# Kernel tuning notes

Measured on AMD Instinct MI355X. Metric: run time of the kernel, lower is better.

Reference implementation:

```python
import jax, jax.numpy as jnp
import numpy as np

N_NODES = 100000
N_EDGES = 1600000
IN_FEATS = 128
HIDDEN = 128
N_CLASSES = 40
EPS = 1e-5  # BatchNorm1d default eps


def setup_inputs():
    key = jax.random.key(0)
    ks = jax.random.split(key, 12)
    s_in = 1.0 / np.sqrt(IN_FEATS)
    s_h = 1.0 / np.sqrt(HIDDEN)
    return {
        "feat": jax.random.normal(ks[0], (N_NODES, IN_FEATS), jnp.float32),
        "src": jax.random.randint(ks[1], (N_EDGES,), 0, N_NODES, jnp.int32),
        "dst": jax.random.randint(ks[2], (N_EDGES,), 0, N_NODES, jnp.int32),
        # GraphConv weights, stored (out, in) as in the torch module
        "w0": jax.random.normal(ks[3], (HIDDEN, IN_FEATS), jnp.float32) * s_in,
        "w1": jax.random.normal(ks[4], (HIDDEN, HIDDEN), jnp.float32) * s_h,
        "w2": jax.random.normal(ks[5], (N_CLASSES, HIDDEN), jnp.float32) * s_h,
        "b2": jnp.zeros((N_CLASSES,), jnp.float32),  # bias only on last layer
        # skip-connection linears (use_linear=True, bias=False)
        "l0": jax.random.normal(ks[6], (HIDDEN, IN_FEATS), jnp.float32) * s_in,
        "l1": jax.random.normal(ks[7], (HIDDEN, HIDDEN), jnp.float32) * s_h,
        "l2": jax.random.normal(ks[8], (N_CLASSES, HIDDEN), jnp.float32) * s_h,
        # BatchNorm affine params for the two hidden layers
        "g0": jnp.ones((HIDDEN,), jnp.float32),
        "beta0": jnp.zeros((HIDDEN,), jnp.float32),
        "g1": jnp.ones((HIDDEN,), jnp.float32),
        "beta1": jnp.zeros((HIDDEN,), jnp.float32),
    }


def _spmm(h, src, dst):
    # copy_u + sum aggregation: out[d] = sum_{e: dst[e]==d} h[src[e]]
    return jax.ops.segment_sum(h[src], dst, num_segments=N_NODES)


def gcn_forward(feat, src, dst, w0, w1, w2, b2, l0, l1, l2, g0, beta0, g1, beta1):
    ones = jnp.ones((src.shape[0],), jnp.float32)
    out_deg = jnp.clip(jax.ops.segment_sum(ones, src, num_segments=N_NODES), 1.0)
    in_deg = jnp.clip(jax.ops.segment_sum(ones, dst, num_segments=N_NODES), 1.0)
    out_norm = out_deg ** -0.5  # norm='both', applied to src features
    in_norm = in_deg ** -0.5    # norm='both', applied to aggregated result

    def conv(h, W, bias, in_gt_out):
        hs = h * out_norm[:, None]
        if in_gt_out:  # in_feats > out_feats: project first, then aggregate
            rst = _spmm(hs @ W.T, src, dst)
        else:          # aggregate first, then project
            rst = _spmm(hs, src, dst) @ W.T
        rst = rst * in_norm[:, None]
        if bias is not None:
            rst = rst + bias
        return rst

    def bn(x, g, b):
        mu = x.mean(0)
        var = x.var(0)  # biased variance, matches BN training-mode normalization
        return (x - mu) * jax.lax.rsqrt(var + EPS) * g + b

    h = feat  # dropout in eval mode = identity
    h = jax.nn.relu(bn(conv(h, w0, None, IN_FEATS > HIDDEN) + h @ l0.T, g0, beta0))
    h = jax.nn.relu(bn(conv(h, w1, None, False) + h @ l1.T, g1, beta1))
    h = conv(h, w2, b2, HIDDEN > N_CLASSES) + h @ l2.T
    return h


def reference(feat, src, dst, w0, w1, w2, b2, l0, l1, l2, g0, beta0, g1, beta1):
    return gcn_forward(feat, src, dst, w0, w1, w2, b2, l0, l1, l2, g0, beta0, g1, beta1)
```

## Files before the change

### kernel.cpp

```cpp
#include <hip/hip_runtime.h>
#include <hip/hip_fp16.h>
#include <cstdint>
#include <cstddef>

#define N_NODES 100000
#define N_EDGES 1600000
#define EPS 1e-5f

typedef _Float16 half8 __attribute__((ext_vector_type(8)));
typedef float floatx4 __attribute__((ext_vector_type(4)));

#define HCH 64
#define HRG 4
#define HBINS 32768
#define HWORDS (HBINS / 2)
#define HCHUNK (N_EDGES / HCH)
#define HCHUNK4 (HCHUNK / 4)

__global__ void k_hist_part(const int* __restrict__ keys, unsigned int* __restrict__ Hpart) {
  __shared__ unsigned int bins[HWORDS];
  int c = blockIdx.x % HCH, r = blockIdx.x / HCH;
  int base = r * HBINS;
  for (int i = threadIdx.x; i < HWORDS; i += 256) bins[i] = 0;
  __syncthreads();
  const int4* k4 = (const int4*)(keys + c * HCHUNK);
  for (int i = threadIdx.x; i < HCHUNK4; i += 256) {
    int4 k = k4[i];
    int a;
    a = k.x - base; if ((unsigned)a < (unsigned)HBINS) atomicAdd(&bins[a >> 1], 1u << ((a & 1) * 16));
    a = k.y - base; if ((unsigned)a < (unsigned)HBINS) atomicAdd(&bins[a >> 1], 1u << ((a & 1) * 16));
    a = k.z - base; if ((unsigned)a < (unsigned)HBINS) atomicAdd(&bins[a >> 1], 1u << ((a & 1) * 16));
    a = k.w - base; if ((unsigned)a < (unsigned)HBINS) atomicAdd(&bins[a >> 1], 1u << ((a & 1) * 16));
  }
  __syncthreads();
  unsigned int* outp = Hpart + ((size_t)blockIdx.x << 14);
  for (int i = threadIdx.x; i < HWORDS; i += 256) outp[i] = bins[i];
}

__global__ void k_hist_scan2(const unsigned short* __restrict__ Hs,
                             unsigned short* __restrict__ Hd,
                             int* __restrict__ degd, float* __restrict__ out_norm,
                             float* __restrict__ in_norm, int* __restrict__ bsum) {
  __shared__ int sred[256];
  int t = threadIdx.x;
  int b = blockIdx.x * 256 + t;
  int total = 0;
  if (b < N_NODES) {
    int r = b >> 15, lo = b & (HBINS - 1);
    const unsigned short* ps = Hs + ((size_t)(r * HCH) << 15) + lo;
    unsigned int ds = 0;
#pragma unroll 8
    for (int c = 0; c < HCH; ++c) ds += ps[(size_t)c << 15];
    unsigned short* pd = Hd + ((size_t)(r * HCH) << 15) + lo;
    unsigned int tt = 0;
#pragma unroll 8
    for (int c = 0; c < HCH; ++c) {
      unsigned int v = pd[(size_t)c << 15];
      pd[(size_t)c << 15] = (unsigned short)tt;
      tt += v;
    }
    total = (int)tt;
    degd[b] = total;
    out_norm[b] = rsqrtf((float)max((int)ds, 1));
    in_norm[b] = rsqrtf((float)max(total, 1));
  }
  sred[t] = total;
  __syncthreads();
  for (int off = 128; off > 0; off >>= 1) {
    if (t < off) sred[t] += sred[t + off];
    __syncthreads();
  }
  if (t == 0) bsum[blockIdx.x] = sred[0];
}

__global__ void k_build(const int* __restrict__ src, const int* __restrict__ dst,
                        const unsigned short* __restrict__ Hbase,
                        const int* __restrict__ row_start, int* __restrict__ col) {
  __shared__ unsigned int cur[HWORDS];
  int c = blockIdx.x % HCH, r = blockIdx.x / HCH;
  int base = r * HBINS;
  for (int i = threadIdx.x; i < HWORDS; i += 256) cur[i] = 0;
  __syncthreads();
  const unsigned short* hb = Hbase + ((size_t)blockIdx.x << 15);
  const int4* d4 = (const int4*)(dst + c * HCHUNK);
  const int4* s4 = (const int4*)(src + c * HCHUNK);
  for (int i = threadIdx.x; i < HCHUNK4; i += 256) {
    int4 d = d4[i];
    int4 s = s4[i];
    int a;
    a = d.x - base;
    if ((unsigned)a < (unsigned)HBINS) {
      unsigned old = atomicAdd(&cur[a >> 1], 1u << ((a & 1) * 16));
      unsigned lr = (old >> ((a & 1) * 16)) & 0xffffu;
      col[row_start[d.x] + hb[a] + lr] = s.x;
    }
    a = d.y - base;
    if ((unsigned)a < (unsigned)HBINS) {
      unsigned old = atomicAdd(&cur[a >> 1], 1u << ((a & 1) * 16));
      unsigned lr = (old >> ((a & 1) * 16)) & 0xffffu;
      col[row_start[d.y] + hb[a] + lr] = s.y;
    }
    a = d.z - base;
    if ((unsigned)a < (unsigned)HBINS) {
      unsigned old = atomicAdd(&cur[a >> 1], 1u << ((a & 1) * 16));
      unsigned lr = (old >> ((a & 1) * 16)) & 0xffffu;
      col[row_start[d.z] + hb[a] + lr] = s.z;
    }
    a = d.w - base;
    if ((unsigned)a < (unsigned)HBINS) {
      unsigned old = atomicAdd(&cur[a >> 1], 1u << ((a & 1) * 16));
      unsigned lr = (old >> ((a & 1) * 16)) & 0xffffu;
      col[row_start[d.w] + hb[a] + lr] = s.w;
    }
  }
}

__global__ void k_scan2(int* bsum, int nb) {
  __shared__ int s[512];
  int t = threadIdx.x;
  int v = (t < nb) ? bsum[t] : 0;
  s[t] = v;
  __syncthreads();
  for (int off = 1; off < 512; off <<= 1) {
    int x = (t >= off) ? s[t - off] : 0;
    __syncthreads();
    s[t] += x;
    __syncthreads();
  }
  if (t < nb) bsum[t] = s[t] - v;
}

__global__ void k_scan3(const int* __restrict__ degd, const int* __restrict__ bsum,
                        int* row_start) {
  __shared__ int s[256];
  int t = threadIdx.x;
  int i = blockIdx.x * 256 + t;
  int v = (i < N_NODES) ? degd[i] : 0;
  s[t] = v;
  __syncthreads();
  for (int off = 1; off < 256; off <<= 1) {
    int x = (t >= off) ? s[t - off] : 0;
    __syncthreads();
    s[t] += x;
    __syncthreads();
  }
  if (i < N_NODES) row_start[i] = bsum[blockIdx.x] + s[t] - v;
  if (i == 0) row_start[N_NODES] = N_EDGES;
}

__global__ void k_w2h(const float* __restrict__ w0, const float* __restrict__ l0,
                      const float* __restrict__ w1, const float* __restrict__ l1,
                      const float* __restrict__ w2, const float* __restrict__ l2,
                      unsigned short* __restrict__ W) {
  int i = blockIdx.x * 256 + threadIdx.x;
  if (i >= 18944) return;
  int h = i * 4;
  const float* src; int off;
  if (h < 16384)      { src = w0; off = h; }
  else if (h < 32768) { src = l0; off = h - 16384; }
  else if (h < 49152) { src = w1; off = h - 32768; }
  else if (h < 65536) { src = l1; off = h - 49152; }
  else if (h < 70656) { src = w2; off = h - 65536; }
  else                { src = l2; off = h - 70656; }
  float4 v = *(const float4*)(src + off);
  ushort4 o;
  o.x = __half_as_ushort(__float2half_rn(v.x));
  o.y = __half_as_ushort(__float2half_rn(v.y));
  o.z = __half_as_ushort(__float2half_rn(v.z));
  o.w = __half_as_ushort(__float2half_rn(v.w));
  ((ushort4*)W)[i] = o;
}

__global__ void k_feat2h(const float* __restrict__ feat, unsigned short* __restrict__ F) {
  int i = blockIdx.x * 256 + threadIdx.x;
  if (i >= N_NODES * 32) return;
  float4 v = ((const float4*)feat)[i];
  ushort4 u;
  u.x = __half_as_ushort(__float2half_rn(v.x));
  u.y = __half_as_ushort(__float2half_rn(v.y));
  u.z = __half_as_ushort(__float2half_rn(v.z));
  u.w = __half_as_ushort(__float2half_rn(v.w));
  ((ushort4*)F)[i] = u;
}

template<int BN>
__global__ void k_agg128h(const unsigned short* __restrict__ X, const int* __restrict__ col,
                          const int* __restrict__ row_start,
                          const float* __restrict__ out_norm,
                          const float* __restrict__ in_norm,
                          const float* __restrict__ stats,
                          const float* __restrict__ g, const float* __restrict__ bb,
                          unsigned short* __restrict__ out16) {
  __shared__ float scA[128], shA[128];
  int t = threadIdx.x;
  if (BN) {
    if (t < 128) {
      const float inv = 1.f / (float)N_NODES;
      float mu = stats[t] * inv;
      float var = stats[128 + t] * inv - mu * mu;
      float s = rsqrtf(var + EPS) * g[t];
      scA[t] = s;
      shA[t] = bb[t] - mu * s;
    }
    __syncthreads();
  }
  int wave = t >> 6;
  int lane = t & 63;
  int node = blockIdx.x * 4 + wave;
  if (node >= N_NODES) return;
  int q = lane >> 4;
  int sub = lane & 15;
  float scR[8], shR[8];
  if (BN) {
#pragma unroll
    for (int j = 0; j < 8; ++j) { scR[j] = scA[sub * 8 + j]; shR[j] = shA[sub * 8 + j]; }
  }
  int s0 = row_start[node], s1 = row_start[node + 1];
  const uint4* hp = (const uint4*)X;
  float a[8];
#pragma unroll
  for (int j = 0; j < 8; ++j) a[j] = 0.f;
  int e = s0 + q;
  for (; e + 4 < s1; e += 8) {
    int c0 = col[e];
    int c1 = col[e + 4];
    float on0 = out_norm[c0];
    float on1 = out_norm[c1];
    uint4 u0 = hp[(size_t)c0 * 16 + sub];
    uint4 u1 = hp[(size_t)c1 * 16 + sub];
    const __half2* h0 = (const __half2*)&u0;
    const __half2* h1 = (const __half2*)&u1;
#pragma unroll
    for (int j = 0; j < 4; ++j) {
      float2 f0 = __half22float2(h0[j]);
      float2 f1 = __half22float2(h1[j]);
      if (BN) {
        f0.x = fmaxf(f0.x * scR[2 * j] + shR[2 * j], 0.f);
        f0.y = fmaxf(f0.y * scR[2 * j + 1] + shR[2 * j + 1], 0.f);
        f1.x = fmaxf(f1.x * scR[2 * j] + shR[2 * j], 0.f);
        f1.y = fmaxf(f1.y * scR[2 * j + 1] + shR[2 * j + 1], 0.f);
      }
      a[2 * j] += on0 * f0.x + on1 * f1.x;
      a[2 * j + 1] += on0 * f0.y + on1 * f1.y;
    }
  }
  if (e < s1) {
    int c = col[e];
    float on = out_norm[c];
    uint4 u = hp[(size_t)c * 16 + sub];
    const __half2* h0 = (const __half2*)&u;
#pragma unroll
    for (int j = 0; j < 4; ++j) {
      float2 f = __half22float2(h0[j]);
      if (BN) {
        f.x = fmaxf(f.x * scR[2 * j] + shR[2 * j], 0.f);
        f.y = fmaxf(f.y * scR[2 * j + 1] + shR[2 * j + 1], 0.f);
      }
      a[2 * j] += on * f.x;
      a[2 * j + 1] += on * f.y;
    }
  }
#pragma unroll
  for (int j = 0; j < 8; ++j) {
    a[j] += __shfl_xor(a[j], 16);
    a[j] += __shfl_xor(a[j], 32);
  }
  if (q == 0) {
    float sc = in_norm[node];
    __half2 o[4];
#pragma unroll
    for (int j = 0; j < 4; ++j)
      o[j] = __float22half2_rn(make_float2(a[2 * j] * sc, a[2 * j + 1] * sc));
    ((uint4*)out16)[(size_t)node * 16 + sub] = *(const uint4*)o;
  }
}

template<int BN>
__launch_bounds__(256)
__global__ void k_gemm_dual16(const unsigned short* __restrict__ Xa,
                              const unsigned short* __restrict__ Xh,
                              const float* __restrict__ stats,
                              const float* __restrict__ g, const float* __restrict__ bb,
                              const unsigned short* __restrict__ W16,
                              unsigned short* __restrict__ Out16, float* __restrict__ pstats) {
  __shared__ __align__(16) unsigned short smem[128 * 136];
  __shared__ float scA[128], shA[128];
  int t = threadIdx.x;
  int row0 = blockIdx.x * 64;
  int w = t >> 6, lane = t & 63;
  int q = lane >> 4, m = lane & 15;
  if (BN && t < 128) {
    const float inv = 1.f / (float)N_NODES;
    float mu = stats[t] * inv;
    float var = stats[128 + t] * inv - mu * mu;
    float s = rsqrtf(var + EPS) * g[t];
    scA[t] = s;
    shA[t] = bb[t] - mu * s;
  }
  size_t arow = (size_t)min(row0 + w * 16 + m, N_NODES - 1);
  floatx4 acc[8];
#pragma unroll
  for (int i = 0; i < 8; ++i) acc[i] = (floatx4){0.f, 0.f, 0.f, 0.f};

  for (int phase = 0; phase < 2; ++phase) {
    const unsigned short* Xg = phase ? Xh : Xa;
    const uint4* xr = (const uint4*)Xg + arow * 16 + q;
    uint4 av[4];
    av[0] = xr[0]; av[1] = xr[4]; av[2] = xr[8]; av[3] = xr[12];
    __syncthreads();
    {
      const uint4* wsrc = (const uint4*)(W16 + ((size_t)phase << 14));
#pragma unroll
      for (int it = 0; it < 8; ++it) {
        int idx = it * 256 + t;
        *(uint4*)&smem[(idx >> 4) * 136 + (idx & 15) * 8] = wsrc[idx];
      }
    }
    if (BN && phase == 1) {
#pragma unroll
      for (int ks = 0; ks < 4; ++ks) {
        int kk = ks * 32 + q * 8;
        __half2* hh = (__half2*)&av[ks];
#pragma unroll
        for (int j = 0; j < 4; ++j) {
          float2 f = __half22float2(hh[j]);
          f.x = fmaxf(f.x * scA[kk + 2 * j] + shA[kk + 2 * j], 0.f);
          f.y = fmaxf(f.y * scA[kk + 2 * j + 1] + shA[kk + 2 * j + 1], 0.f);
          hh[j] = __float22half2_rn(f);
        }
      }
    }
    __syncthreads();
#pragma unroll
    for (int ks = 0; ks < 4; ++ks) {
      half8 a = *(half8*)&av[ks];
      int kk = ks * 32 + q * 8;
#pragma unroll
      for (int t8 = 0; t8 < 8; ++t8) {
        half8 b = *(const half8*)&smem[(t8 * 16 + m) * 136 + kk];
        acc[t8] = __builtin_amdgcn_mfma_f32_16x16x32_f16(a, b, acc[t8], 0, 0, 0);
      }
    }
  }
  float ps[8], pq[8];
#pragma unroll
  for (int t8 = 0; t8 < 8; ++t8) {
    float s = 0.f, sq = 0.f;
#pragma unroll
    for (int i = 0; i < 4; ++i) {
      int row = row0 + w * 16 + q * 4 + i;
      if (row < N_NODES) {
        float v = acc[t8][i];
        s += v; sq += v * v;
      }
    }
    s += __shfl_xor(s, 16);
    s += __shfl_xor(s, 32);
    sq += __shfl_xor(sq, 16);
    sq += __shfl_xor(sq, 32);
    ps[t8] = s; pq[t8] = sq;
  }
  __syncthreads();
  unsigned short* sT = smem;
  float* pSum = (float*)(smem + 8704);
  float* pSq = pSum + 512;
#pragma unroll
  for (int t8 = 0; t8 < 8; ++t8) {
    int c = t8 * 16 + m;
#pragma unroll
    for (int i = 0; i < 4; ++i) {
      int r = w * 16 + q * 4 + i;
      sT[r * 136 + c] = __half_as_ushort(__float2half_rn(acc[t8][i]));
    }
    if (q == 0) {
      pSum[w * 128 + c] = ps[t8];
      pSq[w * 128 + c] = pq[t8];
    }
  }
  __syncthreads();
#pragma unroll
  for (int it = 0; it < 4; ++it) {
    int idx = it * 256 + t;
    int r = idx >> 4, gg = idx & 15;
    int row = row0 + r;
    if (row < N_NODES)
      *(uint4*)&Out16[(size_t)row * 128 + gg * 8] = *(const uint4*)&sT[r * 136 + gg * 8];
  }
  if (t < 128) {
    float s = (pSum[t] + pSum[128 + t]) + (pSum[256 + t] + pSum[384 + t]);
    float sq = (pSq[t] + pSq[128 + t]) + (pSq[256 + t] + pSq[384 + t]);
    pstats[(size_t)blockIdx.x * 256 + t] = s;
    pstats[(size_t)blockIdx.x * 256 + 128 + t] = sq;
  }
}

__global__ void k_stats_red(const float* __restrict__ pstats, float* __restrict__ stats,
                            int nblk) {
  int t = threadIdx.x;
  float s = 0.f;
  for (int b = blockIdx.x; b < nblk; b += gridDim.x)
    s += pstats[(size_t)b * 256 + t];
  atomicAdd(&stats[t], s);
}

__launch_bounds__(256)
__global__ void k_gemm2_16(const unsigned short* __restrict__ X,
                           const float* __restrict__ stats,
                           const float* __restrict__ g, const float* __restrict__ bb,
                           const unsigned short* __restrict__ W80,
                           const float* __restrict__ b2,
                           const float* __restrict__ out_norm,
                           __half* __restrict__ p, float* __restrict__ out) {
  __shared__ __align__(16) unsigned short smem[80 * 136];
  __shared__ float scA[128], shA[128];
  int t = threadIdx.x;
  int row0 = blockIdx.x * 64;
  int w = t >> 6, lane = t & 63;
  int q = lane >> 4, m = lane & 15;
  if (t < 128) {
    const float inv = 1.f / (float)N_NODES;
    float mu = stats[t] * inv;
    float var = stats[128 + t] * inv - mu * mu;
    float s = rsqrtf(var + EPS) * g[t];
    scA[t] = s;
    shA[t] = bb[t] - mu * s;
  }
  size_t arow = (size_t)min(row0 + w * 16 + m, N_NODES - 1);
  const uint4* xr = (const uint4*)X + arow * 16 + q;
  uint4 av[4];
  av[0] = xr[0]; av[1] = xr[4]; av[2] = xr[8]; av[3] = xr[12];
  {
    const uint4* wsrc = (const uint4*)W80;
#pragma unroll
    for (int it = 0; it < 5; ++it) {
      int idx = it * 256 + t;
      *(uint4*)&smem[(idx >> 4) * 136 + (idx & 15) * 8] = wsrc[idx];
    }
  }
  __syncthreads();
#pragma unroll
  for (int ks = 0; ks < 4; ++ks) {
    int kk = ks * 32 + q * 8;
    __half2* hh = (__half2*)&av[ks];
#pragma unroll
    for (int j = 0; j < 4; ++j) {
      float2 f = __half22float2(hh[j]);
      f.x = fmaxf(f.x * scA[kk + 2 * j] + shA[kk + 2 * j], 0.f);
      f.y = fmaxf(f.y * scA[kk + 2 * j + 1] + shA[kk + 2 * j + 1], 0.f);
      hh[j] = __float22half2_rn(f);
    }
  }
  floatx4 acc[5];
#pragma unroll
  for (int i = 0; i < 5; ++i) acc[i] = (floatx4){0.f, 0.f, 0.f, 0.f};
#pragma unroll
  for (int ks = 0; ks < 4; ++ks) {
    half8 a = *(half8*)&av[ks];
    int kk = ks * 32 + q * 8;
#pragma unroll
    for (int t5 = 0; t5 < 5; ++t5) {
      half8 b = *(const half8*)&smem[(t5 * 16 + m) * 136 + kk];
      acc[t5] = __builtin_amdgcn_mfma_f32_16x16x32_f16(a, b, acc[t5], 0, 0, 0);
    }
  }
  __syncthreads();
  unsigned short* sTp = smem;
  float* sTo = (float*)(smem + 4608);
  {
    unsigned int* zp = (unsigned int*)sTp;
    for (int idx = t; idx < 768; idx += 256) {
      int r = idx / 12, wc = 20 + idx % 12;
      zp[r * 36 + wc] = 0u;
    }
  }
  float on4[4];
#pragma unroll
  for (int i = 0; i < 4; ++i) {
    int row = row0 + w * 16 + q * 4 + i;
    on4[i] = out_norm[min(row, N_NODES - 1)];
  }
#pragma unroll
  for (int t5 = 0; t5 < 5; ++t5) {
    int c = t5 * 16 + m;
#pragma unroll
    for (int i = 0; i < 4; ++i) {
      int r = w * 16 + q * 4 + i;
      if (c < 40) {
        sTp[r * 72 + c] = __half_as_ushort(__float2half_rn(on4[i] * acc[t5][i]));
      } else {
        sTo[r * 44 + (c - 40)] = acc[t5][i] + b2[c - 40];
      }
    }
  }
  __syncthreads();
#pragma unroll
  for (int it = 0; it < 2; ++it) {
    int idx = it * 256 + t;
    int r = idx >> 3, gg = idx & 7;
    int row = row0 + r;
    if (row < N_NODES)
      *(uint4*)((unsigned short*)p + (size_t)row * 64 + gg * 8) = *(const uint4*)&sTp[r * 72 + gg * 8];
  }
  for (int it = 0; it < 3; ++it) {
    int idx = it * 256 + t;
    if (idx < 640) {
      int r = idx / 10, gg = idx % 10;
      int row = row0 + r;
      if (row < N_NODES)
        *(float4*)(out + (size_t)row * 40 + gg * 4) = *(const float4*)&sTo[r * 44 + gg * 4];
    }
  }
}

__global__ void k_agg64h(const __half* __restrict__ p, const int* __restrict__ col,
                         const int* __restrict__ row_start,
                         const float* __restrict__ in_norm,
                         float* __restrict__ out) {
  int wave = threadIdx.x >> 6, lane = threadIdx.x & 63;
  int node = blockIdx.x * 4 + wave;
  if (node >= N_NODES) return;
  int oct = lane >> 3;
  int sub = lane & 7;
  int s0 = row_start[node], s1 = row_start[node + 1];
  const uint4* pp = (const uint4*)p;
  float a[8];
#pragma unroll
  for (int j = 0; j < 8; ++j) a[j] = 0.f;
  int e = s0 + oct;
  for (; e + 8 < s1; e += 16) {
    int c0 = col[e];
    int c1 = col[e + 8];
    uint4 u0 = pp[(size_t)c0 * 8 + sub];
    uint4 u1 = pp[(size_t)c1 * 8 + sub];
    const __half2* h0 = (const __half2*)&u0;
    const __half2* h1 = (const __half2*)&u1;
#pragma unroll
    for (int j = 0; j < 4; ++j) {
      float2 f0 = __half22float2(h0[j]);
      float2 f1 = __half22float2(h1[j]);
      a[2 * j] += f0.x + f1.x;
      a[2 * j + 1] += f0.y + f1.y;
    }
  }
  if (e < s1) {
    uint4 u = pp[(size_t)col[e] * 8 + sub];
    const __half2* h0 = (const __half2*)&u;
#pragma unroll
    for (int j = 0; j < 4; ++j) {
      float2 f = __half22float2(h0[j]);
      a[2 * j] += f.x;
      a[2 * j + 1] += f.y;
    }
  }
#pragma unroll
  for (int j = 0; j < 8; ++j) {
    a[j] += __shfl_xor(a[j], 8);
    a[j] += __shfl_xor(a[j], 16);
    a[j] += __shfl_xor(a[j], 32);
  }
  if (oct == 0 && sub < 5) {
    float sc = in_norm[node];
    float4* op = (float4*)(out + (size_t)node * 40 + (size_t)sub * 8);
    float4 v0 = op[0], v1 = op[1];
    v0.x += sc * a[0]; v0.y += sc * a[1]; v0.z += sc * a[2]; v0.w += sc * a[3];
    v1.x += sc * a[4]; v1.y += sc * a[5]; v1.z += sc * a[6]; v1.w += sc * a[7];
    op[0] = v0; op[1] = v1;
  }
}

extern "C" void kernel_launch(void* const* d_in, const int* in_sizes, int n_in,
                              void* d_out, int out_size, void* d_ws, size_t ws_size,
                              hipStream_t stream) {
  const float* feat = (const float*)d_in[0];
  const int* src = (const int*)d_in[1];
  const int* dst = (const int*)d_in[2];
  const float* w0 = (const float*)d_in[3];
  const float* w1 = (const float*)d_in[4];
  const float* w2 = (const float*)d_in[5];
  const float* b2 = (const float*)d_in[6];
  const float* l0 = (const float*)d_in[7];
  const float* l1 = (const float*)d_in[8];
  const float* l2 = (const float*)d_in[9];
  const float* g0 = (const float*)d_in[10];
  const float* beta0 = (const float*)d_in[11];
  const float* g1 = (const float*)d_in[12];
  const float* beta1 = (const float*)d_in[13];
  float* out = (float*)d_out;

  char* ws = (char*)d_ws;
  size_t off = 0;
  auto alloc = [&](size_t bytes) {
    void* ptr = ws + off;
    off = (off + bytes + 255) & ~(size_t)255;
    return ptr;
  };
  unsigned short* A16 = (unsigned short*)alloc(2 * (size_t)N_NODES * 128);
  float* B = (float*)alloc(sizeof(float) * (size_t)N_NODES * 128);
  unsigned short* F = (unsigned short*)alloc(2 * (size_t)N_NODES * 128);
  int* degd = (int*)alloc(sizeof(int) * N_NODES);
  int* row_start = (int*)alloc(sizeof(int) * (N_NODES + 1));
  int* colb = (int*)alloc(sizeof(int) * N_EDGES);
  float* out_norm = (float*)alloc(sizeof(float) * N_NODES);
  float* in_norm = (float*)alloc(sizeof(float) * N_NODES);
  int* bsum = (int*)alloc(sizeof(int) * 512);
  float* stats0 = (float*)alloc(sizeof(float) * 256);
  float* stats1 = (float*)alloc(sizeof(float) * 256);
  unsigned short* W16 = (unsigned short*)alloc(2 * (size_t)75776);
  int gb = (N_NODES + 63) / 64;
  float* pstats = (float*)alloc(sizeof(float) * (size_t)gb * 256);

  unsigned int* Hs = (unsigned int*)B;
  unsigned int* Hd = Hs + (size_t)HCH * HRG * HWORDS;
  unsigned short* P0 = (unsigned short*)B;
  unsigned short* P1 = F;

  int nb = (N_NODES + 255) / 256;
  int hb = HCH * HRG;

  k_w2h<<<74, 256, 0, stream>>>(w0, l0, w1, l1, w2, l2, W16);

  k_hist_part<<<hb, 256, 0, stream>>>(src, Hs);
  k_hist_part<<<hb, 256, 0, stream>>>(dst, Hd);
  k_hist_scan2<<<nb, 256, 0, stream>>>((const unsigned short*)Hs, (unsigned short*)Hd,
                                       degd, out_norm, in_norm, bsum);
  k_scan2<<<1, 512, 0, stream>>>(bsum, nb);
  k_scan3<<<nb, 256, 0, stream>>>(degd, bsum, row_start);
  k_build<<<hb, 256, 0, stream>>>(src, dst, (const unsigned short*)Hd, row_start, colb);

  int ab = (N_NODES + 3) / 4;
  int fb = (N_NODES * 32 + 255) / 256;

  k_feat2h<<<fb, 256, 0, stream>>>(feat, F);
  k_agg128h<0><<<ab, 256, 0, stream>>>(F, colb, row_start, out_norm, in_norm,
                                       nullptr, nullptr, nullptr, A16);
  k_gemm_dual16<0><<<gb, 256, 0, stream>>>(A16, F, nullptr, nullptr, nullptr,
                                           W16, P0, pstats);
  hipMemsetAsync(stats0, 0, sizeof(float) * 256, stream);
  k_stats_red<<<32, 256, 0, stream>>>(pstats, stats0, gb);

  k_agg128h<1><<<ab, 256, 0, stream>>>(P0, colb, row_start, out_norm, in_norm,
                                       stats0, g0, beta0, A16);
  k_gemm_dual16<1><<<gb, 256, 0, stream>>>(A16, P0, stats0, g0, beta0,
                                           W16 + 32768, P1, pstats);
  hipMemsetAsync(stats1, 0, sizeof(float) * 256, stream);
  k_stats_red<<<32, 256, 0, stream>>>(pstats, stats1, gb);

  __half* p = (__half*)A16;
  k_gemm2_16<<<gb, 256, 0, stream>>>(P1, stats1, g1, beta1, W16 + 65536, b2, out_norm, p, out);
  k_agg64h<<<ab, 256, 0, stream>>>(p, colb, row_start, in_norm, out);
}
```

Baseline: 476.5 us.

## Double GEMM row tile and use packed half BN-ReLU in aggregation

```diff
diff --git a/kernel.cpp b/kernel.cpp
--- a/kernel.cpp
+++ b/kernel.cpp
@@ -9,6 +9,15 @@
 
 typedef _Float16 half8 __attribute__((ext_vector_type(8)));
 typedef float floatx4 __attribute__((ext_vector_type(4)));
+
+__device__ inline __half2 bnrelu2(__half2 v, __half2 sc, __half2 sh) {
+  __half2 y = __hfma2(v, sc, sh);
+  unsigned u = *(unsigned*)&y;
+  unsigned keep = (~u) & 0x80008000u;
+  unsigned m = (keep >> 15) * 0xFFFFu;
+  u &= m;
+  return *(__half2*)&u;
+}
 
 #define HCH 64
 #define HRG 4
@@ -191,30 +200,31 @@
                           const float* __restrict__ stats,
                           const float* __restrict__ g, const float* __restrict__ bb,
                           unsigned short* __restrict__ out16) {
-  __shared__ float scA[128], shA[128];
   int t = threadIdx.x;
-  if (BN) {
+  int lane = t & 63;
+  int sub = lane & 15;
+  __half2 scR[4], shR[4];
+  if constexpr (BN) {
+    __shared__ __half hsc[128], hsh[128];
     if (t < 128) {
       const float inv = 1.f / (float)N_NODES;
       float mu = stats[t] * inv;
       float var = stats[128 + t] * inv - mu * mu;
       float s = rsqrtf(var + EPS) * g[t];
-      scA[t] = s;
-      shA[t] = bb[t] - mu * s;
-    }
-    __syncthreads();
+      hsc[t] = __float2half(s);
+      hsh[t] = __float2half(bb[t] - mu * s);
+    }
+    __syncthreads();
+#pragma unroll
+    for (int j = 0; j < 4; ++j) {
+      scR[j] = *(const __half2*)&hsc[sub * 8 + 2 * j];
+      shR[j] = *(const __half2*)&hsh[sub * 8 + 2 * j];
+    }
   }
   int wave = t >> 6;
-  int lane = t & 63;
   int node = blockIdx.x * 4 + wave;
   if (node >= N_NODES) return;
   int q = lane >> 4;
-  int sub = lane & 15;
-  float scR[8], shR[8];
-  if (BN) {
-#pragma unroll
-    for (int j = 0; j < 8; ++j) { scR[j] = scA[sub * 8 + j]; shR[j] = shA[sub * 8 + j]; }
-  }
   int s0 = row_start[node], s1 = row_start[node + 1];
   const uint4* hp = (const uint4*)X;
   float a[8];
@@ -232,14 +242,13 @@
     const __half2* h1 = (const __half2*)&u1;
 #pragma unroll
     for (int j = 0; j < 4; ++j) {
-      float2 f0 = __half22float2(h0[j]);
-      float2 f1 = __half22float2(h1[j]);
-      if (BN) {
-        f0.x = fmaxf(f0.x * scR[2 * j] + shR[2 * j], 0.f);
-        f0.y = fmaxf(f0.y * scR[2 * j + 1] + shR[2 * j + 1], 0.f);
-        f1.x = fmaxf(f1.x * scR[2 * j] + shR[2 * j], 0.f);
-        f1.y = fmaxf(f1.y * scR[2 * j + 1] + shR[2 * j + 1], 0.f);
+      __half2 v0 = h0[j], v1 = h1[j];
+      if constexpr (BN) {
+        v0 = bnrelu2(v0, scR[j], shR[j]);
+        v1 = bnrelu2(v1, scR[j], shR[j]);
       }
+      float2 f0 = __half22float2(v0);
+      float2 f1 = __half22float2(v1);
       a[2 * j] += on0 * f0.x + on1 * f1.x;
       a[2 * j + 1] += on0 * f0.y + on1 * f1.y;
     }
@@ -251,11 +260,9 @@
     const __half2* h0 = (const __half2*)&u;
 #pragma unroll
     for (int j = 0; j < 4; ++j) {
-      float2 f = __half22float2(h0[j]);
-      if (BN) {
-        f.x = fmaxf(f.x * scR[2 * j] + shR[2 * j], 0.f);
-        f.y = fmaxf(f.y * scR[2 * j + 1] + shR[2 * j + 1], 0.f);
-      }
+      __half2 v0 = h0[j];
+      if constexpr (BN) v0 = bnrelu2(v0, scR[j], shR[j]);
+      float2 f = __half22float2(v0);
       a[2 * j] += on * f.x;
       a[2 * j + 1] += on * f.y;
     }
@@ -286,7 +293,7 @@
   __shared__ __align__(16) unsigned short smem[128 * 136];
   __shared__ float scA[128], shA[128];
   int t = threadIdx.x;
-  int row0 = blockIdx.x * 64;
+  int row0 = blockIdx.x * 128;
   int w = t >> 6, lane = t & 63;
   int q = lane >> 4, m = lane & 15;
   if (BN && t < 128) {
@@ -297,16 +304,21 @@
     scA[t] = s;
     shA[t] = bb[t] - mu * s;
   }
-  size_t arow = (size_t)min(row0 + w * 16 + m, N_NODES - 1);
-  floatx4 acc[8];
-#pragma unroll
-  for (int i = 0; i < 8; ++i) acc[i] = (floatx4){0.f, 0.f, 0.f, 0.f};
+  size_t ar0 = (size_t)min(row0 + w * 32 + m, N_NODES - 1);
+  size_t ar1 = (size_t)min(row0 + w * 32 + 16 + m, N_NODES - 1);
+  floatx4 acc[2][8];
+#pragma unroll
+  for (int rt = 0; rt < 2; ++rt)
+#pragma unroll
+    for (int i = 0; i < 8; ++i) acc[rt][i] = (floatx4){0.f, 0.f, 0.f, 0.f};
 
   for (int phase = 0; phase < 2; ++phase) {
     const unsigned short* Xg = phase ? Xh : Xa;
-    const uint4* xr = (const uint4*)Xg + arow * 16 + q;
-    uint4 av[4];
-    av[0] = xr[0]; av[1] = xr[4]; av[2] = xr[8]; av[3] = xr[12];
+    const uint4* xr0 = (const uint4*)Xg + ar0 * 16 + q;
+    const uint4* xr1 = (const uint4*)Xg + ar1 * 16 + q;
+    uint4 av0[4], av1[4];
+    av0[0] = xr0[0]; av0[1] = xr0[4]; av0[2] = xr0[8]; av0[3] = xr0[12];
+    av1[0] = xr1[0]; av1[1] = xr1[4]; av1[2] = xr1[8]; av1[3] = xr1[12];
     __syncthreads();
     {
       const uint4* wsrc = (const uint4*)(W16 + ((size_t)phase << 14));
@@ -320,77 +332,81 @@
 #pragma unroll
       for (int ks = 0; ks < 4; ++ks) {
         int kk = ks * 32 + q * 8;
-        __half2* hh = (__half2*)&av[ks];
+        __half2* hh0 = (__half2*)&av0[ks];
+        __half2* hh1 = (__half2*)&av1[ks];
 #pragma unroll
         for (int j = 0; j < 4; ++j) {
-          float2 f = __half22float2(hh[j]);
-          f.x = fmaxf(f.x * scA[kk + 2 * j] + shA[kk + 2 * j], 0.f);
-          f.y = fmaxf(f.y * scA[kk + 2 * j + 1] + shA[kk + 2 * j + 1], 0.f);
-          hh[j] = __float22half2_rn(f);
+          float sc = scA[kk + 2 * j], sc1 = scA[kk + 2 * j + 1];
+          float sh = shA[kk + 2 * j], sh1 = shA[kk + 2 * j + 1];
+          float2 f0 = __half22float2(hh0[j]);
+          float2 f1 = __half22float2(hh1[j]);
+          f0.x = fmaxf(f0.x * sc + sh, 0.f);
+          f0.y = fmaxf(f0.y * sc1 + sh1, 0.f);
+          f1.x = fmaxf(f1.x * sc + sh, 0.f);
+          f1.y = fmaxf(f1.y * sc1 + sh1, 0.f);
+          hh0[j] = __float22half2_rn(f0);
+          hh1[j] = __float22half2_rn(f1);
         }
       }
     }
     __syncthreads();
 #pragma unroll
     for (int ks = 0; ks < 4; ++ks) {
-      half8 a = *(half8*)&av[ks];
+      half8 a0 = *(half8*)&av0[ks];
+      half8 a1 = *(half8*)&av1[ks];
       int kk = ks * 32 + q * 8;
 #pragma unroll
       for (int t8 = 0; t8 < 8; ++t8) {
         half8 b = *(const half8*)&smem[(t8 * 16 + m) * 136 + kk];
-        acc[t8] = __builtin_amdgcn_mfma_f32_16x16x32_f16(a, b, acc[t8], 0, 0, 0);
+        acc[0][t8] = __builtin_amdgcn_mfma_f32_16x16x32_f16(a0, b, acc[0][t8], 0, 0, 0);
+        acc[1][t8] = __builtin_amdgcn_mfma_f32_16x16x32_f16(a1, b, acc[1][t8], 0, 0, 0);
       }
     }
   }
-  float ps[8], pq[8];
 #pragma unroll
   for (int t8 = 0; t8 < 8; ++t8) {
     float s = 0.f, sq = 0.f;
 #pragma unroll
-    for (int i = 0; i < 4; ++i) {
-      int row = row0 + w * 16 + q * 4 + i;
-      if (row < N_NODES) {
-        float v = acc[t8][i];
-        s += v; sq += v * v;
+    for (int rt = 0; rt < 2; ++rt)
+#pragma unroll
+      for (int i = 0; i < 4; ++i) {
+        int row = row0 + w * 32 + rt * 16 + q * 4 + i;
+        if (row < N_NODES) {
+          float v = acc[rt][t8][i];
+          s += v; sq += v * v;
+        }
       }
-    }
     s += __shfl_xor(s, 16);
     s += __shfl_xor(s, 32);
     sq += __shfl_xor(sq, 16);
     sq += __shfl_xor(sq, 32);
-    ps[t8] = s; pq[t8] = sq;
+    if (q == 0) {
+      int c = t8 * 16 + m;
+      pstats[((size_t)blockIdx.x * 4 + w) * 256 + c] = s;
+      pstats[((size_t)blockIdx.x * 4 + w) * 256 + 128 + c] = sq;
+    }
   }
   __syncthreads();
   unsigned short* sT = smem;
-  float* pSum = (float*)(smem + 8704);
-  float* pSq = pSum + 512;
 #pragma unroll
   for (int t8 = 0; t8 < 8; ++t8) {
     int c = t8 * 16 + m;
 #pragma unroll
-    for (int i = 0; i < 4; ++i) {
-      int r = w * 16 + q * 4 + i;
-      sT[r * 136 + c] = __half_as_ushort(__float2half_rn(acc[t8][i]));
-    }
-    if (q == 0) {
-      pSum[w * 128 + c] = ps[t8];
-      pSq[w * 128 + c] = pq[t8];
-    }
-  }
-  __syncthreads();
-#pragma unroll
-  for (int it = 0; it < 4; ++it) {
+    for (int rt = 0; rt < 2; ++rt)
+#pragma unroll
+      for (int i = 0; i < 4; ++i) {
+        int r = w * 32 + rt * 16 + q * 4 + i;
+        sT[r * 136 + c] = __half_as_ushort(__float2half_rn(acc[rt][t8][i]));
+      }
+  }
+  __syncthreads();
+#pragma unroll
+  for (int it = 0; it < 8; ++it) {
     int idx = it * 256 + t;
     int r = idx >> 4, gg = idx & 15;
     int row = row0 + r;
     if (row < N_NODES)
       *(uint4*)&Out16[(size_t)row * 128 + gg * 8] = *(const uint4*)&sT[r * 136 + gg * 8];
-  }
-  if (t < 128) {
-    float s = (pSum[t] + pSum[128 + t]) + (pSum[256 + t] + pSum[384 + t]);
-    float sq = (pSq[t] + pSq[128 + t]) + (pSq[256 + t] + pSq[384 + t]);
-    pstats[(size_t)blockIdx.x * 256 + t] = s;
-    pstats[(size_t)blockIdx.x * 256 + 128 + t] = sq;
   }
 }
 
@@ -606,8 +622,10 @@
   float* stats0 = (float*)alloc(sizeof(float) * 256);
   float* stats1 = (float*)alloc(sizeof(float) * 256);
   unsigned short* W16 = (unsigned short*)alloc(2 * (size_t)75776);
-  int gb = (N_NODES + 63) / 64;
-  float* pstats = (float*)alloc(sizeof(float) * (size_t)gb * 256);
+  int gb2 = (N_NODES + 127) / 128;
+  int nstat = gb2 * 4;
+  float* pstats = (float*)alloc(sizeof(float) * (size_t)nstat * 256);
+  int gb64 = (N_NODES + 63) / 64;
 
   unsigned int* Hs = (unsigned int*)B;
   unsigned int* Hd = Hs + (size_t)HCH * HRG * HWORDS;
@@ -633,19 +651,19 @@
   k_feat2h<<<fb, 256, 0, stream>>>(feat, F);
   k_agg128h<0><<<ab, 256, 0, stream>>>(F, colb, row_start, out_norm, in_norm,
                                        nullptr, nullptr, nullptr, A16);
-  k_gemm_dual16<0><<<gb, 256, 0, stream>>>(A16, F, nullptr, nullptr, nullptr,
-                                           W16, P0, pstats);
+  k_gemm_dual16<0><<<gb2, 256, 0, stream>>>(A16, F, nullptr, nullptr, nullptr,
+                                            W16, P0, pstats);
   hipMemsetAsync(stats0, 0, sizeof(float) * 256, stream);
-  k_stats_red<<<32, 256, 0, stream>>>(pstats, stats0, gb);
+  k_stats_red<<<32, 256, 0, stream>>>(pstats, stats0, nstat);
 
   k_agg128h<1><<<ab, 256, 0, stream>>>(P0, colb, row_start, out_norm, in_norm,
                                        stats0, g0, beta0, A16);
-  k_gemm_dual16<1><<<gb, 256, 0, stream>>>(A16, P0, stats0, g0, beta0,
-                                           W16 + 32768, P1, pstats);
+  k_gemm_dual16<1><<<gb2, 256, 0, stream>>>(A16, P0, stats0, g0, beta0,
+                                            W16 + 32768, P1, pstats);
   hipMemsetAsync(stats1, 0, sizeof(float) * 256, stream);
-  k_stats_red<<<32, 256, 0, stream>>>(pstats, stats1, gb);
+  k_stats_red<<<32, 256, 0, stream>>>(pstats, stats1, nstat);
 
   __half* p = (__half*)A16;
-  k_gemm2_16<<<gb, 256, 0, stream>>>(P1, stats1, g1, beta1, W16 + 65536, b2, out_norm, p, out);
+  k_gemm2_16<<<gb64, 256, 0, stream>>>(P1, stats1, g1, beta1, W16 + 65536, b2, out_norm, p, out);
   k_agg64h<<<ab, 256, 0, stream>>>(p, colb, row_start, in_norm, out);
 }
```

After: 520.7 us. 9.3% more time.
